# Performance work log

Measured on AMD Instinct MI355X. Metric: run time of the kernel, lower is better.

The kernel has to match this reference:

```python
import jax, jax.numpy as jnp
import numpy as np

N, E = 50000, 600000
D_IN, HID, CLS = 128, 128, 64
TEM = (0.9, 0.8)  # tem[0], tem[1] from init


def setup_inputs() -> dict:
    key = jax.random.key(0)
    ks = jax.random.split(key, 20)
    def lin(k, fan_in, shape):
        return (jax.random.normal(k, shape, jnp.float32) / np.float32(np.sqrt(fan_in)))
    return {
        "features": jax.random.normal(ks[0], (N, D_IN), jnp.float32),
        "src1": jax.random.randint(ks[1], (E,), 0, N, jnp.int32),
        "dst1": jax.random.randint(ks[2], (E,), 0, N, jnp.int32),
        "src2": jax.random.randint(ks[3], (E,), 0, N, jnp.int32),
        "dst2": jax.random.randint(ks[4], (E,), 0, N, jnp.int32),
        "W1": lin(ks[5], D_IN, (D_IN, HID)),
        "b1": jnp.zeros((HID,), jnp.float32),
        "W2": lin(ks[6], HID, (HID, CLS)),
        "b2": jnp.zeros((CLS,), jnp.float32),
        "Wg11": lin(ks[7], 2 * HID, (2 * HID, 1)),
        "bg11": jnp.zeros((1,), jnp.float32),
        "Wg12": lin(ks[8], 2 * HID, (2 * HID, 1)),
        "bg12": jnp.zeros((1,), jnp.float32),
        "Wg21": lin(ks[9], 2 * CLS, (2 * CLS, 1)),
        "bg21": jnp.zeros((1,), jnp.float32),
        "Wg22": lin(ks[10], 2 * CLS, (2 * CLS, 1)),
        "bg22": jnp.zeros((1,), jnp.float32),
    }


def _gin(x, src, dst, W, b):
    # DGL GINConv, aggregator='sum', eps=0: apply_func(x + sum_{u->v} x_u)
    agg = jax.ops.segment_sum(x[src], dst, num_segments=N)  # [N, d]
    return (x + agg) @ W + b


def _gate_scale(a, c, Wg, bg):
    # ga = softmax(Linear(cat[a,c]), dim=1): [N,1] -> all ones (size-1 axis)
    # torch.diag of [N,1] matrix -> its single diagonal element [0,0]
    g = jnp.concatenate([a, c], axis=1) @ Wg + bg  # [N, 1]
    g = jax.nn.softmax(g, axis=1)
    return g[0, 0]  # scalar (dropout is identity in eval mode)


def reference(features, src1, dst1, src2, dst2, W1, b1, W2, b2,
              Wg11, bg11, Wg12, bg12, Wg21, bg21, Wg22, bg22):
    # layer 1 on both graphs (no ELU in the two-graph branch, per source)
    x11 = _gin(features, src1, dst1, W1, b1)
    x12 = _gin(features, src2, dst2, W1, b1)
    x12 = TEM[1] * _gate_scale(x11, x12, Wg11, bg11) * x12
    x11 = TEM[0] * _gate_scale(x12, x11, Wg12, bg12) * x11
    x1 = x11 + x12
    # layer 2 on both graphs
    x21 = _gin(x1, src1, dst1, W2, b2)
    x22 = _gin(x1, src2, dst2, W2, b2)
    x22 = TEM[1] * _gate_scale(x21, x22, Wg21, bg21) * x22
    x21 = TEM[0] * _gate_scale(x22, x21, Wg22, bg22) * x21
    return x21 + x22
```

## Files before the change

kernel.cpp:

```cpp
#include <hip/hip_runtime.h>

#define N_NODES 50000
#define N_EDGES 600000
#define D 128
#define NCLS 64

#define BIN_SHIFT 9
#define BIN_ROWS 512
#define NBINS 196
#define BIN_CAP 8192
#define CHUNK 4096
#define EPT (CHUNK / 256)

__device__ inline unsigned short f2bf(float f) {
  unsigned int u = __float_as_uint(f);
  unsigned int r = (u + 0x7FFF + ((u >> 16) & 1)) >> 16;
  return (unsigned short)r;
}
__device__ inline float bf2f(unsigned short b) {
  return __uint_as_float(((unsigned int)b) << 16);
}


__global__ __launch_bounds__(256) void ms_scatter(const int* __restrict__ src1,
                                                  const int* __restrict__ dst1,
                                                  const int* __restrict__ src2,
                                                  const int* __restrict__ dst2,
                                                  int* __restrict__ bincnt,
                                                  int2* __restrict__ binbuf) {
  __shared__ int bcnt[NBINS];
  __shared__ int boff[NBINS];
  __shared__ int gbase[NBINS];
  __shared__ int stmp[256];
  __shared__ int2 stage[CHUNK];

  int base = blockIdx.x * CHUNK;
  int nloc = min(CHUNK, 2 * N_EDGES - base);

  for (int t = threadIdx.x; t < NBINS; t += 256) bcnt[t] = 0;
  __syncthreads();

  int rows[EPT], srcs[EPT], bins[EPT];
#pragma unroll
  for (int k = 0; k < EPT; ++k) {
    int t = threadIdx.x + k * 256;
    rows[k] = -1;
    if (t < nloc) {
      int i = base + t;
      int row, sv;
      if (i < N_EDGES) { row = dst1[i]; sv = src1[i]; }
      else { int e = i - N_EDGES; row = N_NODES + dst2[e]; sv = src2[e]; }
      rows[k] = row; srcs[k] = sv;
      bins[k] = row >> BIN_SHIFT;
      atomicAdd(&bcnt[bins[k]], 1);
    }
  }
  __syncthreads();
  {
    int tid = threadIdx.x;
    int v = (tid < NBINS) ? bcnt[tid] : 0;
    stmp[tid] = v;
    __syncthreads();
    int x = v;
    for (int o = 1; o < 256; o <<= 1) {
      int y = (tid >= o) ? stmp[tid - o] : 0;
      __syncthreads();
      x += y;
      stmp[tid] = x;
      __syncthreads();
    }
    if (tid < NBINS) boff[tid] = x - v;
  }
  __syncthreads();
  for (int t = threadIdx.x; t < NBINS; t += 256) {
    gbase[t] = bcnt[t];
    bcnt[t] = boff[t];
  }
  __syncthreads();
#pragma unroll
  for (int k = 0; k < EPT; ++k) {
    if (rows[k] >= 0) {
      int p = atomicAdd(&bcnt[bins[k]], 1);
      stage[p] = make_int2(rows[k], srcs[k]);
    }
  }
  __syncthreads();
  for (int t = threadIdx.x; t < NBINS; t += 256) {
    int c = gbase[t];
    if (c > 0) gbase[t] = atomicAdd(&bincnt[t], c);
  }
  __syncthreads();
  for (int j = threadIdx.x; j < nloc; j += 256) {
    int2 e = stage[j];
    int b = e.x >> BIN_SHIFT;
    int gp = gbase[b] + (j - boff[b]);
    if (gp < BIN_CAP) binbuf[(size_t)b * BIN_CAP + gp] = e;
  }
}


__global__ void scan_bins(const int* __restrict__ bincnt, int* __restrict__ binbase,
                          int* __restrict__ off) {
  __shared__ int sh[256];
  int tid = threadIdx.x;
  int v = (tid < NBINS) ? bincnt[tid] : 0;
  sh[tid] = v;
  __syncthreads();
  int x = v;
  for (int o = 1; o < 256; o <<= 1) {
    int y = (tid >= o) ? sh[tid - o] : 0;
    __syncthreads();
    x += y;
    sh[tid] = x;
    __syncthreads();
  }
  if (tid < NBINS) binbase[tid] = x - v;
  if (tid == 255) off[2 * N_NODES] = x;
}


__global__ __launch_bounds__(512) void bin_build(const int* __restrict__ bincnt,
                                                 const int* __restrict__ binbase,
                                                 const int2* __restrict__ binbuf,
                                                 int* __restrict__ off, int* __restrict__ adj) {
  __shared__ int sh[BIN_ROWS];
  __shared__ int lp[BIN_ROWS];
  int b = blockIdx.x;
  int tid = threadIdx.x;
  int n = min(bincnt[b], BIN_CAP);
  int base = binbase[b];

  sh[tid] = 0;
  __syncthreads();
  for (int t = tid; t < n; t += 512) {
    int row = binbuf[(size_t)b * BIN_CAP + t].x;
    atomicAdd(&sh[row & (BIN_ROWS - 1)], 1);
  }
  __syncthreads();
  int v = sh[tid];
  int x = v;
  for (int o = 1; o < BIN_ROWS; o <<= 1) {
    int y = (tid >= o) ? sh[tid - o] : 0;
    __syncthreads();
    x += y;
    sh[tid] = x;
    __syncthreads();
  }
  lp[tid] = x - v;
  int row = (b << BIN_SHIFT) + tid;
  if (row < 2 * N_NODES) off[row] = base + lp[tid];
  __syncthreads();
  sh[tid] = lp[tid];
  __syncthreads();
  for (int t = tid; t < n; t += 512) {
    int2 e = binbuf[(size_t)b * BIN_CAP + t];
    int p = atomicAdd(&sh[e.x & (BIN_ROWS - 1)], 1);
    adj[base + p] = e.y;
  }
}


__global__ void w12_kernel(const float* __restrict__ W1, const float* __restrict__ W2,
                           const float* __restrict__ b1,
                           float* __restrict__ W12, float* __restrict__ c) {
  int o = blockIdx.x * blockDim.x + threadIdx.x;
  int i = o >> 6, j = o & 63;
  float s = 0.f;
  for (int k = 0; k < D; ++k) s += W1[i * D + k] * W2[k * NCLS + j];
  W12[i * NCLS + j] = s;
  if (o < NCLS) {
    float t = 0.f;
    for (int k = 0; k < D; ++k) t += b1[k] * W2[k * NCLS + o];
    c[o] = t;
  }
}


__global__ __launch_bounds__(256) void gemm64_kernel(const float* __restrict__ A,
                                                     const float* __restrict__ W,
                                                     unsigned short* __restrict__ C, int M) {
  constexpr int BM = 64, BK = 16, BN = 64;
  constexpr int TCOL = BN / 16;
  __shared__ float As[BK][BM + 1];
  __shared__ float Ws[BK][BN];
  const int tx = threadIdx.x & 15;
  const int ty = threadIdx.x >> 4;
  const int row0 = blockIdx.x * BM;
  float acc[4][TCOL];
#pragma unroll
  for (int r = 0; r < 4; ++r)
#pragma unroll
    for (int c = 0; c < TCOL; ++c) acc[r][c] = 0.f;

  for (int k0 = 0; k0 < D; k0 += BK) {
    {
      int t = threadIdx.x;
      int r = t >> 2;
      int kq = (t & 3) << 2;
      int gr = row0 + r;
      float4 v = make_float4(0.f, 0.f, 0.f, 0.f);
      if (gr < M) v = *(const float4*)(A + (size_t)gr * D + k0 + kq);
      As[kq + 0][r] = v.x;
      As[kq + 1][r] = v.y;
      As[kq + 2][r] = v.z;
      As[kq + 3][r] = v.w;
    }
    {
      int k = threadIdx.x >> 4;
      int c4 = (threadIdx.x & 15) << 2;
      *(float4*)(&Ws[k][c4]) = *(const float4*)(W + (size_t)(k0 + k) * BN + c4);
    }
    __syncthreads();
#pragma unroll
    for (int k = 0; k < BK; ++k) {
      float a[4];
#pragma unroll
      for (int r = 0; r < 4; ++r) a[r] = As[k][ty * 4 + r];
      float w[TCOL];
#pragma unroll
      for (int c = 0; c < TCOL; ++c) w[c] = Ws[k][tx * TCOL + c];
#pragma unroll
      for (int r = 0; r < 4; ++r)
#pragma unroll
        for (int c = 0; c < TCOL; ++c) acc[r][c] += a[r] * w[c];
    }
    __syncthreads();
  }
#pragma unroll
  for (int r = 0; r < 4; ++r) {
    int gr = row0 + ty * 4 + r;
    if (gr < M) {
      ushort4 pk;
      pk.x = f2bf(acc[r][0]);
      pk.y = f2bf(acc[r][1]);
      pk.z = f2bf(acc[r][2]);
      pk.w = f2bf(acc[r][3]);
      *(ushort4*)(C + (size_t)gr * BN + tx * TCOL) = pk;
    }
  }
}


template <int FIN, int OUT_BF16>
__global__ __launch_bounds__(256) void agg64_kernel(const unsigned short* __restrict__ X,
                                                    const int* __restrict__ off,
                                                    const int* __restrict__ adj,
                                                    const float* __restrict__ cvec,
                                                    const float* __restrict__ b2,
                                                    void* __restrict__ Yv) {
  int wid = (blockIdx.x * blockDim.x + threadIdx.x) >> 6;
  if (wid >= N_NODES) return;
  int lane = threadIdx.x & 63;

  float self = bf2f(X[(size_t)wid * 64 + lane]);

  int s1 = off[wid], e1 = off[wid + 1];
  int s2 = off[N_NODES + wid], e2 = off[N_NODES + wid + 1];

  float acc[2];
#pragma unroll
  for (int g = 0; g < 2; ++g) {
    int s = g ? s2 : s1, e = g ? e2 : e1;
    float a0 = 0.f, a1 = 0.f, a2 = 0.f, a3 = 0.f;
    for (int base = s; base < e; base += 64) {
      int m = e - base;
      if (m > 64) m = 64;
      int idx = (lane < m) ? adj[base + lane] : 0;
      int i = 0;
      for (; i + 4 <= m; i += 4) {
        int n0 = __shfl(idx, i + 0);
        int n1 = __shfl(idx, i + 1);
        int n2 = __shfl(idx, i + 2);
        int n3 = __shfl(idx, i + 3);
        float f0 = bf2f(X[(size_t)n0 * 64 + lane]);
        float f1 = bf2f(X[(size_t)n1 * 64 + lane]);
        float f2 = bf2f(X[(size_t)n2 * 64 + lane]);
        float f3 = bf2f(X[(size_t)n3 * 64 + lane]);
        a0 += f0; a1 += f1; a2 += f2; a3 += f3;
      }
      for (; i < m; ++i) {
        int n0 = __shfl(idx, i);
        a0 += bf2f(X[(size_t)n0 * 64 + lane]);
      }
    }
    acc[g] = (a0 + a1) + (a2 + a3);
  }
  float y = 1.7f * self + 0.9f * acc[0] + 0.8f * acc[1];
  if (FIN) {
    float sv = 1.7f * (1.7f + 0.9f * (float)(e1 - s1) + 0.8f * (float)(e2 - s2));
    y += sv * cvec[lane] + 1.7f * b2[lane];
  }
  if (OUT_BF16) {
    ((unsigned short*)Yv)[(size_t)wid * 64 + lane] = f2bf(y);
  } else {
    ((float*)Yv)[(size_t)wid * 64 + lane] = y;
  }
}


extern "C" void kernel_launch(void* const* d_in, const int* in_sizes, int n_in,
                              void* d_out, int out_size, void* d_ws, size_t ws_size,
                              hipStream_t stream) {
  const float* F  = (const float*)d_in[0];
  const int* src1 = (const int*)d_in[1];
  const int* dst1 = (const int*)d_in[2];
  const int* src2 = (const int*)d_in[3];
  const int* dst2 = (const int*)d_in[4];
  const float* W1 = (const float*)d_in[5];
  const float* b1 = (const float*)d_in[6];
  const float* W2 = (const float*)d_in[7];
  const float* b2 = (const float*)d_in[8];
  float* out = (float*)d_out;

  char* ws = (char*)d_ws;
  auto aln = [](size_t x) { return (x + 255) & ~(size_t)255; };
  size_t o = 0;
  int* bincnt  = (int*)(ws + o); o = aln(o + (size_t)NBINS * 4);
  int* binbase = (int*)(ws + o); o = aln(o + (size_t)NBINS * 4);
  int* off     = (int*)(ws + o); o = aln(o + ((size_t)2 * N_NODES + 1) * 4);
  int2* binbuf = (int2*)(ws + o); o = aln(o + (size_t)NBINS * BIN_CAP * 8);
  int* adj     = (int*)(ws + o); o = aln(o + (size_t)2 * N_EDGES * 4);
  float* W12   = (float*)(ws + o); o = aln(o + (size_t)D * NCLS * 4);
  float* cvec  = (float*)(ws + o); o = aln(o + NCLS * 4);
  unsigned short* H = (unsigned short*)(ws + o); o = aln(o + (size_t)N_NODES * NCLS * 2);
  unsigned short* T = (unsigned short*)(ws + o); o = aln(o + (size_t)N_NODES * NCLS * 2);
  (void)ws_size;

  hipMemsetAsync(bincnt, 0, (size_t)NBINS * 4, stream);
  ms_scatter<<<(2 * N_EDGES + CHUNK - 1) / CHUNK, 256, 0, stream>>>(src1, dst1, src2, dst2,
                                                                    bincnt, binbuf);
  scan_bins<<<1, 256, 0, stream>>>(bincnt, binbase, off);
  bin_build<<<NBINS, 512, 0, stream>>>(bincnt, binbase, binbuf, off, adj);

  w12_kernel<<<32, 256, 0, stream>>>(W1, W2, b1, W12, cvec);
  gemm64_kernel<<<(N_NODES + 63) / 64, 256, 0, stream>>>(F, W12, H, N_NODES);
  agg64_kernel<0, 1><<<N_NODES / 4, 256, 0, stream>>>(H, off, adj, cvec, b2, T);
  agg64_kernel<1, 0><<<N_NODES / 4, 256, 0, stream>>>(T, off, adj, cvec, b2, out);
}
```

Baseline: 232.7 us.

## Fuse kernels horizontally to cut launches: scatter with W12, scan+build with GEMM

The W1·W2 weight-product computation moves into extra blocks of the edge-scatter kernel. The global bin scan is folded into each bin-build block, recomputed redundantly from bincnt. The feature GEMM runs as extra blocks of the build kernel. This cuts the launch count from seven to four and lets independent work share the GPU. In exchange, the GEMM blocks run with 512 threads of which only 256 work, and combined shared memory per block grows, which may reduce occupancy.

```diff
diff --git a/kernel.cpp b/kernel.cpp
--- a/kernel.cpp
+++ b/kernel.cpp
@@ -11,6 +11,8 @@
 #define BIN_CAP 8192
 #define CHUNK 4096
 #define EPT (CHUNK / 256)
+#define NCHUNKS 293
+#define W12_BLOCKS 17
 
 __device__ inline unsigned short f2bf(float f) {
   unsigned int u = __float_as_uint(f);
@@ -22,17 +24,40 @@
 }
 
 
-__global__ __launch_bounds__(256) void ms_scatter(const int* __restrict__ src1,
-                                                  const int* __restrict__ dst1,
-                                                  const int* __restrict__ src2,
-                                                  const int* __restrict__ dst2,
-                                                  int* __restrict__ bincnt,
-                                                  int2* __restrict__ binbuf) {
+__global__ __launch_bounds__(256) void scatter_w12(const int* __restrict__ src1,
+                                                   const int* __restrict__ dst1,
+                                                   const int* __restrict__ src2,
+                                                   const int* __restrict__ dst2,
+                                                   int* __restrict__ bincnt,
+                                                   int2* __restrict__ binbuf,
+                                                   const float* __restrict__ W1,
+                                                   const float* __restrict__ W2,
+                                                   const float* __restrict__ b1,
+                                                   float* __restrict__ W12,
+                                                   float* __restrict__ cvec) {
   __shared__ int bcnt[NBINS];
   __shared__ int boff[NBINS];
   __shared__ int gbase[NBINS];
   __shared__ int stmp[256];
   __shared__ int2 stage[CHUNK];
+
+  if (blockIdx.x >= NCHUNKS) {
+    int gid = (blockIdx.x - NCHUNKS) * 256 + threadIdx.x;
+    for (int t = gid; t < D * NCLS + NCLS; t += W12_BLOCKS * 256) {
+      if (t < D * NCLS) {
+        int i = t >> 6, j = t & 63;
+        float s = 0.f;
+        for (int k = 0; k < D; ++k) s += W1[i * D + k] * W2[k * NCLS + j];
+        W12[t] = s;
+      } else {
+        int j = t - D * NCLS;
+        float s = 0.f;
+        for (int k = 0; k < D; ++k) s += b1[k] * W2[k * NCLS + j];
+        cvec[j] = s;
+      }
+    }
+    return;
+  }
 
   int base = blockIdx.x * CHUNK;
   int nloc = min(CHUNK, 2 * N_EDGES - base);
@@ -99,93 +124,71 @@
 }
 
 
-__global__ void scan_bins(const int* __restrict__ bincnt, int* __restrict__ binbase,
-                          int* __restrict__ off) {
-  __shared__ int sh[256];
-  int tid = threadIdx.x;
-  int v = (tid < NBINS) ? bincnt[tid] : 0;
-  sh[tid] = v;
-  __syncthreads();
-  int x = v;
-  for (int o = 1; o < 256; o <<= 1) {
-    int y = (tid >= o) ? sh[tid - o] : 0;
-    __syncthreads();
-    x += y;
-    sh[tid] = x;
-    __syncthreads();
-  }
-  if (tid < NBINS) binbase[tid] = x - v;
-  if (tid == 255) off[2 * N_NODES] = x;
-}
-
-
-__global__ __launch_bounds__(512) void bin_build(const int* __restrict__ bincnt,
-                                                 const int* __restrict__ binbase,
-                                                 const int2* __restrict__ binbuf,
-                                                 int* __restrict__ off, int* __restrict__ adj) {
+__global__ __launch_bounds__(512) void build_gemm(const int* __restrict__ bincnt,
+                                                  const int2* __restrict__ binbuf,
+                                                  int* __restrict__ off, int* __restrict__ adj,
+                                                  const float* __restrict__ A,
+                                                  const float* __restrict__ W,
+                                                  unsigned short* __restrict__ C) {
   __shared__ int sh[BIN_ROWS];
   __shared__ int lp[BIN_ROWS];
-  int b = blockIdx.x;
+  __shared__ int stmp[256];
+  __shared__ float As[16][65];
+  __shared__ float Ws[16][64];
+
   int tid = threadIdx.x;
-  int n = min(bincnt[b], BIN_CAP);
-  int base = binbase[b];
-
-  sh[tid] = 0;
-  __syncthreads();
-  for (int t = tid; t < n; t += 512) {
-    int row = binbuf[(size_t)b * BIN_CAP + t].x;
-    atomicAdd(&sh[row & (BIN_ROWS - 1)], 1);
-  }
-  __syncthreads();
-  int v = sh[tid];
-  int x = v;
-  for (int o = 1; o < BIN_ROWS; o <<= 1) {
-    int y = (tid >= o) ? sh[tid - o] : 0;
-    __syncthreads();
-    x += y;
-    sh[tid] = x;
-    __syncthreads();
-  }
-  lp[tid] = x - v;
-  int row = (b << BIN_SHIFT) + tid;
-  if (row < 2 * N_NODES) off[row] = base + lp[tid];
-  __syncthreads();
-  sh[tid] = lp[tid];
-  __syncthreads();
-  for (int t = tid; t < n; t += 512) {
-    int2 e = binbuf[(size_t)b * BIN_CAP + t];
-    int p = atomicAdd(&sh[e.x & (BIN_ROWS - 1)], 1);
-    adj[base + p] = e.y;
-  }
-}
-
-
-__global__ void w12_kernel(const float* __restrict__ W1, const float* __restrict__ W2,
-                           const float* __restrict__ b1,
-                           float* __restrict__ W12, float* __restrict__ c) {
-  int o = blockIdx.x * blockDim.x + threadIdx.x;
-  int i = o >> 6, j = o & 63;
-  float s = 0.f;
-  for (int k = 0; k < D; ++k) s += W1[i * D + k] * W2[k * NCLS + j];
-  W12[i * NCLS + j] = s;
-  if (o < NCLS) {
-    float t = 0.f;
-    for (int k = 0; k < D; ++k) t += b1[k] * W2[k * NCLS + o];
-    c[o] = t;
-  }
-}
-
-
-__global__ __launch_bounds__(256) void gemm64_kernel(const float* __restrict__ A,
-                                                     const float* __restrict__ W,
-                                                     unsigned short* __restrict__ C, int M) {
+
+  if (blockIdx.x < NBINS) {
+    int b = blockIdx.x;
+    if (tid < 256) stmp[tid] = (tid < NBINS) ? bincnt[tid] : 0;
+    __syncthreads();
+    int x = (tid < 256) ? stmp[tid] : 0;
+    for (int o = 1; o < 256; o <<= 1) {
+      int y = (tid < 256 && tid >= o) ? stmp[tid - o] : 0;
+      __syncthreads();
+      x += y;
+      if (tid < 256) stmp[tid] = x;
+      __syncthreads();
+    }
+    int base = (b == 0) ? 0 : stmp[b - 1];
+    if (b == 0 && tid == 0) off[2 * N_NODES] = stmp[NBINS - 1];
+    int n = min(bincnt[b], BIN_CAP);
+
+    sh[tid] = 0;
+    __syncthreads();
+    for (int t = tid; t < n; t += 512) {
+      int row = binbuf[(size_t)b * BIN_CAP + t].x;
+      atomicAdd(&sh[row & (BIN_ROWS - 1)], 1);
+    }
+    __syncthreads();
+    int v = sh[tid];
+    int xx = v;
+    for (int o = 1; o < BIN_ROWS; o <<= 1) {
+      int y = (tid >= o) ? sh[tid - o] : 0;
+      __syncthreads();
+      xx += y;
+      sh[tid] = xx;
+      __syncthreads();
+    }
+    lp[tid] = xx - v;
+    int row = (b << BIN_SHIFT) + tid;
+    if (row < 2 * N_NODES) off[row] = base + lp[tid];
+    __syncthreads();
+    sh[tid] = lp[tid];
+    __syncthreads();
+    for (int t = tid; t < n; t += 512) {
+      int2 e = binbuf[(size_t)b * BIN_CAP + t];
+      int p = atomicAdd(&sh[e.x & (BIN_ROWS - 1)], 1);
+      adj[base + p] = e.y;
+    }
+    return;
+  }
+
   constexpr int BM = 64, BK = 16, BN = 64;
   constexpr int TCOL = BN / 16;
-  __shared__ float As[BK][BM + 1];
-  __shared__ float Ws[BK][BN];
-  const int tx = threadIdx.x & 15;
-  const int ty = threadIdx.x >> 4;
-  const int row0 = blockIdx.x * BM;
+  const int tx = tid & 15;
+  const int ty = (tid >> 4) & 15;
+  const int row0 = (blockIdx.x - NBINS) * BM;
   float acc[4][TCOL];
 #pragma unroll
   for (int r = 0; r < 4; ++r)
@@ -193,49 +196,52 @@
     for (int c = 0; c < TCOL; ++c) acc[r][c] = 0.f;
 
   for (int k0 = 0; k0 < D; k0 += BK) {
-    {
-      int t = threadIdx.x;
-      int r = t >> 2;
-      int kq = (t & 3) << 2;
+    if (tid < 256) {
+      int r = tid >> 2;
+      int kq = (tid & 3) << 2;
       int gr = row0 + r;
       float4 v = make_float4(0.f, 0.f, 0.f, 0.f);
-      if (gr < M) v = *(const float4*)(A + (size_t)gr * D + k0 + kq);
+      if (gr < N_NODES) v = *(const float4*)(A + (size_t)gr * D + k0 + kq);
       As[kq + 0][r] = v.x;
       As[kq + 1][r] = v.y;
       As[kq + 2][r] = v.z;
       As[kq + 3][r] = v.w;
     }
-    {
-      int k = threadIdx.x >> 4;
-      int c4 = (threadIdx.x & 15) << 2;
+    if (tid < 256) {
+      int k = tid >> 4;
+      int c4 = (tid & 15) << 2;
       *(float4*)(&Ws[k][c4]) = *(const float4*)(W + (size_t)(k0 + k) * BN + c4);
     }
     __syncthreads();
-#pragma unroll
-    for (int k = 0; k < BK; ++k) {
-      float a[4];
-#pragma unroll
-      for (int r = 0; r < 4; ++r) a[r] = As[k][ty * 4 + r];
-      float w[TCOL];
-#pragma unroll
-      for (int c = 0; c < TCOL; ++c) w[c] = Ws[k][tx * TCOL + c];
-#pragma unroll
-      for (int r = 0; r < 4; ++r)
-#pragma unroll
-        for (int c = 0; c < TCOL; ++c) acc[r][c] += a[r] * w[c];
-    }
-    __syncthreads();
-  }
-#pragma unroll
-  for (int r = 0; r < 4; ++r) {
-    int gr = row0 + ty * 4 + r;
-    if (gr < M) {
-      ushort4 pk;
-      pk.x = f2bf(acc[r][0]);
-      pk.y = f2bf(acc[r][1]);
-      pk.z = f2bf(acc[r][2]);
-      pk.w = f2bf(acc[r][3]);
-      *(ushort4*)(C + (size_t)gr * BN + tx * TCOL) = pk;
+    if (tid < 256) {
+#pragma unroll
+      for (int k = 0; k < BK; ++k) {
+        float a[4];
+#pragma unroll
+        for (int r = 0; r < 4; ++r) a[r] = As[k][ty * 4 + r];
+        float w[TCOL];
+#pragma unroll
+        for (int c = 0; c < TCOL; ++c) w[c] = Ws[k][tx * TCOL + c];
+#pragma unroll
+        for (int r = 0; r < 4; ++r)
+#pragma unroll
+          for (int c = 0; c < TCOL; ++c) acc[r][c] += a[r] * w[c];
+      }
+    }
+    __syncthreads();
+  }
+  if (tid < 256) {
+#pragma unroll
+    for (int r = 0; r < 4; ++r) {
+      int gr = row0 + ty * 4 + r;
+      if (gr < N_NODES) {
+        ushort4 pk;
+        pk.x = f2bf(acc[r][0]);
+        pk.y = f2bf(acc[r][1]);
+        pk.z = f2bf(acc[r][2]);
+        pk.w = f2bf(acc[r][3]);
+        *(ushort4*)(C + (size_t)gr * BN + tx * TCOL) = pk;
+      }
     }
   }
 }
@@ -316,7 +322,6 @@
   auto aln = [](size_t x) { return (x + 255) & ~(size_t)255; };
   size_t o = 0;
   int* bincnt  = (int*)(ws + o); o = aln(o + (size_t)NBINS * 4);
-  int* binbase = (int*)(ws + o); o = aln(o + (size_t)NBINS * 4);
   int* off     = (int*)(ws + o); o = aln(o + ((size_t)2 * N_NODES + 1) * 4);
   int2* binbuf = (int2*)(ws + o); o = aln(o + (size_t)NBINS * BIN_CAP * 8);
   int* adj     = (int*)(ws + o); o = aln(o + (size_t)2 * N_EDGES * 4);
@@ -327,13 +332,10 @@
   (void)ws_size;
 
   hipMemsetAsync(bincnt, 0, (size_t)NBINS * 4, stream);
-  ms_scatter<<<(2 * N_EDGES + CHUNK - 1) / CHUNK, 256, 0, stream>>>(src1, dst1, src2, dst2,
-                                                                    bincnt, binbuf);
-  scan_bins<<<1, 256, 0, stream>>>(bincnt, binbase, off);
-  bin_build<<<NBINS, 512, 0, stream>>>(bincnt, binbase, binbuf, off, adj);
-
-  w12_kernel<<<32, 256, 0, stream>>>(W1, W2, b1, W12, cvec);
-  gemm64_kernel<<<(N_NODES + 63) / 64, 256, 0, stream>>>(F, W12, H, N_NODES);
+  scatter_w12<<<NCHUNKS + W12_BLOCKS, 256, 0, stream>>>(src1, dst1, src2, dst2,
+                                                        bincnt, binbuf, W1, W2, b1, W12, cvec);
+  build_gemm<<<NBINS + (N_NODES + 63) / 64, 512, 0, stream>>>(bincnt, binbuf, off, adj,
+                                                              F, W12, H);
   agg64_kernel<0, 1><<<N_NODES / 4, 256, 0, stream>>>(H, off, adj, cvec, b2, T);
   agg64_kernel<1, 0><<<N_NODES / 4, 256, 0, stream>>>(T, off, adj, cvec, b2, out);
 }
```

Result: faster. 211.2 us (-9.2%).
